# Optimization experiments

Hardware: AMD Instinct MI355X
Metric: run time of the kernel (lower is better)

## Reference

```python
import jax, jax.numpy as jnp
import numpy as np

L, B, DM, H, HID, NSPK, NB, NC, WIN = 128, 64, 1024, 256, 256, 2, 30, 6, 10
F = 2 * H            # biLSTM output feature dim
MEM = F + HID        # concat of node features and graph-conv output
R = 2 * NSPK * NSPK  # number of edge relations


def _build_edges():
    src_l, dst_l = [], []
    for j in range(L):
        for k in range(max(0, j - WIN), min(L, j + WIN + 1)):
            dst_l.append(j); src_l.append(k)
    dst = np.asarray(dst_l, np.int32); src = np.asarray(src_l, np.int32)
    offs = (np.arange(B, dtype=np.int32) * L)[:, None]
    edge_dst = (dst[None] + offs).reshape(-1)
    edge_src = (src[None] + offs).reshape(-1)
    mask = np.zeros((L, L), bool); mask[dst, src] = True
    return edge_src, edge_dst, mask


def setup_inputs():
    key = jax.random.key(0)
    ks = iter(jax.random.split(key, 32))
    rn = lambda *s: jax.random.normal(next(ks), s, jnp.float32) * 0.05
    edge_src, edge_dst, edge_mask = _build_edges()
    return {
        'U': jax.random.normal(next(ks), (L, B, DM), jnp.float32),
        'umask': jnp.ones((B, L), jnp.float32),
        'Wih0': rn(2, 4 * H, DM), 'Whh0': rn(2, 4 * H, H), 'b0': rn(2, 4 * H),
        'Wih1': rn(2, 4 * H, F), 'Whh1': rn(2, 4 * H, H), 'b1': rn(2, 4 * H),
        'W_scalar': rn(F, L),
        'basis': rn(NB, F, HID), 'comp': rn(R, NB),
        'W_root': rn(F, HID), 'b_rgcn': rn(HID),
        'gc_W1': rn(HID, HID), 'gc_W2': rn(HID, HID), 'gc_b': rn(HID),
        'Wm': rn(MEM, MEM), 'bm': rn(MEM),
        'Wl': rn(MEM, HID), 'bl': rn(HID),
        'Ws': rn(HID, NC), 'bs': rn(NC),
        'speakers': jax.random.randint(next(ks), (L, B), 0, NSPK, jnp.int32),
        'edge_src': jnp.asarray(edge_src), 'edge_dst': jnp.asarray(edge_dst),
        'edge_mask': jnp.asarray(edge_mask),
    }


def _lstm_dir(x, Wih, Whh, b, reverse):
    Bx, Hh = x.shape[1], Whh.shape[1]
    def step(carry, xt):
        h, c = carry
        g = xt @ Wih.T + h @ Whh.T + b          # PyTorch gate order i,f,g,o
        i, f, gg, o = jnp.split(g, 4, axis=-1)
        c = jax.nn.sigmoid(f) * c + jax.nn.sigmoid(i) * jnp.tanh(gg)
        h = jax.nn.sigmoid(o) * jnp.tanh(c)
        return (h, c), h
    init = (jnp.zeros((Bx, Hh), x.dtype), jnp.zeros((Bx, Hh), x.dtype))
    return jax.lax.scan(step, init, x, reverse=reverse)[1]


def _bilstm(x, Wih, Whh, b):
    return jnp.concatenate([_lstm_dir(x, Wih[0], Whh[0], b[0], False),
                            _lstm_dir(x, Wih[1], Whh[1], b[1], True)], -1)


def reference(U, umask, Wih0, Whh0, b0, Wih1, Whh1, b1, W_scalar, basis, comp,
              W_root, b_rgcn, gc_W1, gc_W2, gc_b, Wm, bm, Wl, bl, Ws, bs,
              speakers, edge_src, edge_dst, edge_mask):
    # --- 2-layer biLSTM encoder ---
    feats = _bilstm(_bilstm(U, Wih0, Whh0, b0), Wih1, Whh1, b1)   # (L,B,F)
    # --- MaskedEdgeAttention ('attn1'): edge weights ---
    scale = jnp.einsum('sbd,dm->sbm', feats, W_scalar)            # (L,B,L)
    alpha = jax.nn.softmax(scale, axis=0).transpose(1, 2, 0)      # (B,Lt,Ls)
    masked = alpha * jnp.where(edge_mask, 1.0, 1e-10)
    scores = masked / masked.sum(-1, keepdims=True) * edge_mask
    b_idx = edge_dst // L; i0 = edge_dst % L; i1 = edge_src % L
    edge_norm = scores[b_idx, i0, i1]                             # (E,)
    # --- edge types: speaker pair + temporal direction ---
    s_dst = speakers[i0, b_idx]; s_src = speakers[i1, b_idx]
    e_dir = jnp.where(i0 < i1, 0, 1)
    edge_type = s_dst * (2 * NSPK) + s_src * 2 + e_dir            # (E,) in [0,R)
    # --- node features, conversation-major ---
    x = feats.transpose(1, 0, 2).reshape(B * L, F)                # (N,F)
    N = B * L
    # --- RGCNConv with basis decomposition ---
    W_rel = jnp.einsum('rb,bfo->rfo', comp, basis)                # (R,F,HID)
    x_rel = jnp.einsum('nf,rfo->nro', x, W_rel)                   # (N,R,HID)
    msg = x_rel[edge_src, edge_type] * edge_norm[:, None]
    h = jax.ops.segment_sum(msg, edge_dst, num_segments=N) + x @ W_root + b_rgcn
    # --- GraphConv ---
    agg = jax.ops.segment_sum(h[edge_src], edge_dst, num_segments=N)
    h2 = h @ gc_W1 + gc_b + agg @ gc_W2                           # (N,HID)
    em = jnp.concatenate([x, h2], -1)                             # (N,MEM)
    em = em.reshape(B, L, MEM).transpose(1, 0, 2)                 # (L,B,MEM)
    # --- MatchingAttention ('general2') at every timestep, vectorized ---
    um = umask.T                                                  # (L,B)
    x_tr = em @ Wm + bm                                           # (L,B,MEM)
    logits = jnp.einsum('tbm,sbm->tbs', x_tr, em * um[:, :, None]) * umask[None]
    a = jax.nn.softmax(jnp.tanh(logits), axis=2) * umask[None]
    a = a / a.sum(2, keepdims=True)
    att = jnp.einsum('tbs,sbm->tbm', a, em)
    hidden = jax.nn.relu(att @ Wl + bl)                           # dropout = eval identity
    logp = jax.nn.log_softmax(hidden @ Ws + bs, axis=2)           # (L,B,NC)
    return logp.transpose(1, 0, 2).reshape(B * L, NC)
```

## Files before the change

### kernel.cpp

```cpp
#include <hip/hip_runtime.h>
#include <cstdint>


typedef __attribute__((ext_vector_type(8))) short bf16x8;
typedef __attribute__((ext_vector_type(4))) float f32x4;

__device__ __forceinline__ void gload_lds16(const void* g, void* l) {
  __builtin_amdgcn_global_load_lds(
      (const __attribute__((address_space(1))) void*)g,
      (__attribute__((address_space(3))) void*)l, 16, 0, 0);
}

template<bool HASBIAS, bool ACCUM, bool RELU, bool OUTBF>
__global__ __launch_bounds__(256) void gemm_bf16_nt(
    const ushort* __restrict__ A, const ushort* __restrict__ Bt,
    const float* __restrict__ bias, void* __restrict__ Cv,
    int M, int N, int K, long sA, long sB, long sC, long sBias)
{
  const int bz = blockIdx.z;
  A += (long)bz * sA;
  Bt += (long)bz * sB;
  if (HASBIAS) bias += (long)bz * sBias;
  float*  Cf = OUTBF ? nullptr : ((float*)Cv + (long)bz * sC);
  ushort* Cb = OUTBF ? ((ushort*)Cv + (long)bz * sC) : nullptr;

  const int bn = blockIdx.x * 128, bm = blockIdx.y * 128;

  __shared__ ushort As[128][32];
  __shared__ ushort Bs[128][32];

  const int tid = threadIdx.x;
  const int wave = tid >> 6, lane = tid & 63;
  const int wm = (wave >> 1) * 64, wn = (wave & 1) * 64;
  const int fr = lane & 15;
  const int fk = (lane >> 4) * 8;

  f32x4 acc[4][4];
#pragma unroll
  for (int i = 0; i < 4; ++i)
#pragma unroll
    for (int j = 0; j < 4; ++j) acc[i][j] = (f32x4){0.f, 0.f, 0.f, 0.f};

  const int f0 = wave * 2 * 64 + lane;
  const int f1 = f0 + 64;
  const int r0 = f0 >> 2, c0 = (f0 & 3) * 8;
  const int r1 = f1 >> 2, c1 = (f1 & 3) * 8;
  ushort* As0 = (ushort*)As + wave * 2 * 512;
  ushort* As1 = As0 + 512;
  ushort* Bs0 = (ushort*)Bs + wave * 2 * 512;
  ushort* Bs1 = Bs0 + 512;

  for (int k0 = 0; k0 < K; k0 += 32) {
    gload_lds16(A + (long)(bm + r0) * K + k0 + c0, As0);
    gload_lds16(A + (long)(bm + r1) * K + k0 + c1, As1);
    gload_lds16(Bt + (long)(bn + r0) * K + k0 + c0, Bs0);
    gload_lds16(Bt + (long)(bn + r1) * K + k0 + c1, Bs1);
    __syncthreads();

    bf16x8 af[4], bfr[4];
#pragma unroll
    for (int f = 0; f < 4; ++f) {
      af[f]  = *(const bf16x8*)&As[wm + f * 16 + fr][fk];
      bfr[f] = *(const bf16x8*)&Bs[wn + f * 16 + fr][fk];
    }
#pragma unroll
    for (int mf = 0; mf < 4; ++mf)
#pragma unroll
      for (int nf = 0; nf < 4; ++nf)
        acc[mf][nf] = __builtin_amdgcn_mfma_f32_16x16x32_bf16(
            af[mf], bfr[nf], acc[mf][nf], 0, 0, 0);
    __syncthreads();
  }

  float bv[4];
#pragma unroll
  for (int nf = 0; nf < 4; ++nf)
    bv[nf] = HASBIAS ? bias[bn + wn + nf * 16 + fr] : 0.f;

  const int crow0 = (lane >> 4) * 4;
#pragma unroll
  for (int mf = 0; mf < 4; ++mf)
#pragma unroll
    for (int r = 0; r < 4; ++r) {
      const long roff = (long)(bm + wm + mf * 16 + crow0 + r) * N + bn + wn;
#pragma unroll
      for (int nf = 0; nf < 4; ++nf) {
        float v = acc[mf][nf][r] + bv[nf];
        if (OUTBF) {
          unsigned u = __float_as_uint(v);
          u += 0x7fffu + ((u >> 16) & 1u);
          Cb[roff + nf * 16 + fr] = (ushort)(u >> 16);
        } else {
          if (ACCUM) v += Cf[roff + nf * 16 + fr];
          if (RELU) v = fmaxf(v, 0.f);
          Cf[roff + nf * 16 + fr] = v;
        }
      }
    }
}

__device__ __forceinline__ unsigned short f2bf(float f) {
  unsigned u = __float_as_uint(f);
  u += 0x7fffu + ((u >> 16) & 1u);
  return (unsigned short)(u >> 16);
}
__device__ __forceinline__ float bf2f(ushort v) {
  return __uint_as_float(((unsigned)v) << 16);
}
__device__ __forceinline__ float fast_sig(float x) {
  return __builtin_amdgcn_rcpf(1.f + __expf(-x));
}
__device__ __forceinline__ float fast_tanh(float x) {
  return 2.f * fast_sig(2.f * x) - 1.f;
}

__device__ __forceinline__ int sdot4_(uint a, uint b, int c) {
#if __has_builtin(__builtin_amdgcn_sdot4)
  return __builtin_amdgcn_sdot4((int)a, (int)b, c, false);
#else
  int r = c;
  r += ((int)(a << 24) >> 24) * ((int)(b << 24) >> 24);
  r += ((int)(a << 16) >> 24) * ((int)(b << 16) >> 24);
  r += ((int)(a << 8)  >> 24) * ((int)(b << 8)  >> 24);
  r += ((int)a >> 24)         * ((int)b >> 24);
  return r;
#endif
}

__global__ __launch_bounds__(256) void cvt_all_k(
    const float* __restrict__ U, ushort* __restrict__ ubf,
    const float* __restrict__ W0, ushort* __restrict__ w0,
    const float* __restrict__ W1, ushort* __restrict__ w1)
{
  const int bid = blockIdx.x;
  const float* src; ushort* dst; long base;
  if (bid < 8192)       { src = U;  dst = ubf; base = (long)bid * 1024; }
  else if (bid < 10240) { src = W0; dst = w0;  base = (long)(bid - 8192) * 1024; }
  else                  { src = W1; dst = w1;  base = (long)(bid - 10240) * 1024; }
  const long i = base + threadIdx.x * 4;
  float4 v = *(const float4*)(src + i);
  ushort4 o;
  o.x = f2bf(v.x); o.y = f2bf(v.y); o.z = f2bf(v.z); o.w = f2bf(v.w);
  *(ushort4*)(dst + i) = o;
}

__global__ __launch_bounds__(256) void tp_all_k(
    const float* __restrict__ s0, ushort* __restrict__ d0,
    const float* __restrict__ s1, ushort* __restrict__ d1,
    const float* __restrict__ s2, ushort* __restrict__ d2,
    const float* __restrict__ s3, ushort* __restrict__ d3,
    const float* __restrict__ s4, ushort* __restrict__ d4,
    const float* __restrict__ s5, ushort* __restrict__ d5)
{
  __shared__ float tile[32][33];
  const int bid = blockIdx.x;
  const float* src; ushort* dst; int R, C, gx, local;
  if (bid < 128)       { src = s0; dst = d0; R = 512; C = 256; gx = 8;  local = bid; }
  else if (bid < 192)  { src = s1; dst = d1; R = 256; C = 256; gx = 8;  local = bid - 128; }
  else if (bid < 256)  { src = s2; dst = d2; R = 256; C = 256; gx = 8;  local = bid - 192; }
  else if (bid < 832)  { src = s3; dst = d3; R = 768; C = 768; gx = 24; local = bid - 256; }
  else if (bid < 1024) { src = s4; dst = d4; R = 768; C = 256; gx = 8;  local = bid - 832; }
  else                 { src = s5; dst = d5; R = 512; C = 128; gx = 4;  local = bid - 1024; }
  const int c0 = (local % gx) * 32, r0 = (local / gx) * 32;
  const int tx = threadIdx.x & 31, ty = threadIdx.x >> 5;
#pragma unroll
  for (int j = 0; j < 4; ++j)
    tile[ty + j * 8][tx] = src[(long)(r0 + ty + j * 8) * C + c0 + tx];
  __syncthreads();
#pragma unroll
  for (int j = 0; j < 4; ++j)
    dst[(long)(c0 + ty + j * 8) * R + r0 + tx] = f2bf(tile[tx][ty + j * 8]);
}

__global__ __launch_bounds__(256) void pack_whh_all_k(
    const float* __restrict__ Whh0, const float* __restrict__ Whh1,
    uint* __restrict__ Wq, float* __restrict__ fscale)
{
  const int wid = (blockIdx.x * 256 + threadIdx.x) >> 6;
  const int lane = threadIdx.x & 63;
  const int l = wid >> 11;
  const int wid2 = wid & 2047;
  const int d = wid2 >> 10, gi = wid2 & 1023;
  const float* Whh = l ? Whh1 : Whh0;
  const float* row = Whh + ((long)d * 1024 + gi) * 256 + lane * 4;
  float v0 = row[0], v1 = row[1], v2 = row[2], v3 = row[3];
  float am = fmaxf(fmaxf(fabsf(v0), fabsf(v1)), fmaxf(fabsf(v2), fabsf(v3)));
#pragma unroll
  for (int off = 32; off > 0; off >>= 1) am = fmaxf(am, __shfl_xor(am, off, 64));
  am = fmaxf(am, 1e-12f);
  const float inv = 127.f / am;
  int q0 = __float2int_rn(v0 * inv), q1 = __float2int_rn(v1 * inv);
  int q2 = __float2int_rn(v2 * inv), q3 = __float2int_rn(v3 * inv);
  uint w = (uint)(q0 & 255) | ((uint)(q1 & 255) << 8) |
           ((uint)(q2 & 255) << 16) | ((uint)(q3 & 255) << 24);
  Wq[(long)l * 131072 + ((long)d * 64 + lane) * 1024 + gi] = w;
  if (lane == 0) fscale[l * 2048 + d * 1024 + gi] = am / 127.f;
}

__global__ __launch_bounds__(1024) void lstm4_k(
    const float* __restrict__ Xg,
    const uint* __restrict__ Wq,
    const float* __restrict__ fscale,
    ushort* __restrict__ out,
    int bmajor)
{
  const int bx = blockIdx.x;
  const int d = bx >> 6, b = bx & 63;
  const int tid = threadIdx.x;

  __shared__ uint hq[2][64];
  __shared__ float preactF[1024];

  uint w[64];
  const uint* wrow = Wq + (long)d * 65536 + tid;
#pragma unroll
  for (int k4 = 0; k4 < 64; ++k4) w[k4] = wrow[k4 * 1024];

  if (tid < 128) ((uint*)hq)[tid] = 0u;

  const float fsc = fscale[d * 1024 + tid] * (1.0f / 127.0f);
  const float* Xd = Xg + (long)d * 8192 * 1024;

  float c = 0.f;
  float x0 = 0.f, x1 = 0.f, x2 = 0.f, x3 = 0.f;
  if (tid < 256) {
    const float* xr = Xd + ((long)((d ? 127 : 0) * 64 + b)) * 1024;
    x0 = xr[tid]; x1 = xr[tid + 256]; x2 = xr[tid + 512]; x3 = xr[tid + 768];
  }
  __syncthreads();

  int cur = 0;
  for (int step = 0; step < 128; ++step) {
    const int t = d ? 127 - step : step;

    float n0 = 0.f, n1 = 0.f, n2 = 0.f, n3 = 0.f;
    if (tid < 256 && step + 1 < 128) {
      const float* xr = Xd + ((long)((d ? 126 - step : step + 1) * 64 + b)) * 1024;
      n0 = xr[tid]; n1 = xr[tid + 256]; n2 = xr[tid + 512]; n3 = xr[tid + 768];
    }

    int acc = 0;
    const uint4* hrow = (const uint4*)hq[cur];
#pragma unroll
    for (int k16 = 0; k16 < 16; ++k16) {
      uint4 h4 = hrow[k16];
      acc = sdot4_(w[k16 * 4 + 0], h4.x, acc);
      acc = sdot4_(w[k16 * 4 + 1], h4.y, acc);
      acc = sdot4_(w[k16 * 4 + 2], h4.z, acc);
      acc = sdot4_(w[k16 * 4 + 3], h4.w, acc);
    }
    preactF[tid] = (float)acc * fsc;
    __syncthreads();

    if (tid < 256) {
      float p0 = x0 + preactF[tid];
      float p1 = x1 + preactF[tid + 256];
      float p2 = x2 + preactF[tid + 512];
      float p3 = x3 + preactF[tid + 768];
      const float ig = fast_sig(p0), fg = fast_sig(p1);
      const float gg = fast_tanh(p2), og = fast_sig(p3);
      c = fg * c + ig * gg;
      const float h = og * fast_tanh(c);
      const long row = bmajor ? ((long)b * 128 + t) : ((long)t * 64 + b);
      out[row * 512 + (d << 8) + tid] = f2bf(h);
      ((char*)hq[cur ^ 1])[tid] = (char)__float2int_rn(h * 127.f);
      x0 = n0; x1 = n1; x2 = n2; x3 = n3;
    }
    __syncthreads();
    cur ^= 1;
  }
}

__global__ __launch_bounds__(256) void wrel_k(const float* __restrict__ basis,
                                              const float* __restrict__ comp,
                                              ushort* __restrict__ wrel2t) {
  const int f = blockIdx.x;
  const int o = threadIdx.x;
  __shared__ float cs[240];
  if (o < 240) cs[o] = comp[o];
  __syncthreads();
  float acc[8];
#pragma unroll
  for (int r = 0; r < 8; ++r) acc[r] = 0.f;
  for (int bb = 0; bb < 30; ++bb) {
    const float v = basis[((long)bb * 512 + f) * 256 + o];
#pragma unroll
    for (int r = 0; r < 8; ++r) acc[r] = fmaf(cs[r * 30 + bb], v, acc[r]);
  }
#pragma unroll
  for (int r = 0; r < 8; ++r)
    wrel2t[((long)(r * 256 + o)) * 512 + f] = f2bf(acc[r]);
}

__global__ __launch_bounds__(256) void rgcn_fused_k(
    const float* __restrict__ scale, const ushort* __restrict__ xrel,
    const float* __restrict__ hroot, const int* __restrict__ spk,
    ushort* __restrict__ hbf)
{
  const int n = blockIdx.x;
  const int b = n >> 7, t = n & 127;
  const int o = threadIdx.x;
  const int lo = max(t - 10, 0), hi = min(t + 10, 127);
  const int cnt = hi - lo + 1;

  __shared__ float sc[128], red[128];
  __shared__ int spks[21];
  __shared__ int spkt_s;

  if (o < 128) {
    const float v = scale[((long)(b * 128 + o)) * 128 + t];
    sc[o] = v; red[o] = v;
  }
  if (o == 0) spkt_s = spk[t * 64 + b];
  if (o >= 128 && o - 128 < cnt) spks[o - 128] = spk[(lo + o - 128) * 64 + b];
  __syncthreads();
  for (int off = 64; off > 0; off >>= 1) {
    if (o < off) red[o] = fmaxf(red[o], red[o + off]);
    __syncthreads();
  }
  const float m = red[0];
  __syncthreads();
  if (o < 128) {
    const float e = expf(sc[o] - m);
    sc[o] = e;
    const int dd = o - t;
    const bool inwin = (dd <= 10) && (dd >= -10);
    red[o] = e * (inwin ? 1.0f : 1e-10f);
  }
  __syncthreads();
  for (int off = 64; off > 0; off >>= 1) {
    if (o < off) red[o] += red[o + off];
    __syncthreads();
  }
  const float inv_msum = 1.0f / red[0];
  __syncthreads();

  const int spkt = spkt_s;
  float acc = hroot[(long)n * 256 + o];
  for (int q = 0; q < cnt; ++q) {
    const int s = lo + q;
    const float wv = sc[s] * inv_msum;
    const int et = spkt * 4 + spks[q] * 2 + ((t < s) ? 0 : 1);
    acc = fmaf(bf2f(xrel[(((long)(b * 128 + s)) * 8 + et) * 256 + o]), wv, acc);
  }
  hbf[(long)n * 256 + o] = f2bf(acc);
}

__global__ __launch_bounds__(256) void agg_k(const ushort* __restrict__ hbf,
                                             ushort* __restrict__ aggbf) {
  const int n = blockIdx.x;
  const int b = n >> 7, t = n & 127;
  const int o = threadIdx.x;
  const int lo = max(t - 10, 0), hi = min(t + 10, 127);
  float acc = 0.f;
  for (int s = lo; s <= hi; ++s) acc += bf2f(hbf[((long)(b * 128 + s)) * 256 + o]);
  aggbf[(long)n * 256 + o] = f2bf(acc);
}

__global__ __launch_bounds__(256) void em_k(const ushort* __restrict__ xbf,
                                            const float* __restrict__ h2,
                                            ushort* __restrict__ embf) {
  const int n = blockIdx.x;
  const int tid = threadIdx.x;
  embf[(long)n * 768 + tid] = xbf[(long)n * 512 + tid];
  embf[(long)n * 768 + 256 + tid] = xbf[(long)n * 512 + 256 + tid];
  embf[(long)n * 768 + 512 + tid] = f2bf(h2[(long)n * 256 + tid]);
}

__global__ __launch_bounds__(256) void emt_k(const ushort* __restrict__ src,
                                             ushort* __restrict__ dst) {
  __shared__ ushort tile[32][33];
  const int c0 = blockIdx.x * 32;
  const int r0 = blockIdx.y * 32;
  const int b = blockIdx.z;
  const ushort* s = src + (long)b * 98304;
  ushort* d = dst + (long)b * 98304;
  const int tx = threadIdx.x & 31, ty = threadIdx.x >> 5;
#pragma unroll
  for (int j = 0; j < 4; ++j)
    tile[ty + j * 8][tx] = s[(long)(r0 + ty + j * 8) * 768 + c0 + tx];
  __syncthreads();
#pragma unroll
  for (int j = 0; j < 4; ++j)
    d[(long)(c0 + ty + j * 8) * 128 + r0 + tx] = tile[tx][ty + j * 8];
}

__global__ __launch_bounds__(128) void match_softmax_k(const float* __restrict__ logits,
                                                       const float* __restrict__ umask,
                                                       ushort* __restrict__ abf) {
  const int bx = blockIdx.x;
  const int b = bx >> 7;
  const int s = threadIdx.x;
  __shared__ float red[128];
  const float* row = logits + (long)bx * 128;
  const float um = umask[b * 128 + s];
  const float v = tanhf(row[s] * um * um);
  red[s] = v; __syncthreads();
  for (int off = 64; off > 0; off >>= 1) { if (s < off) red[s] = fmaxf(red[s], red[s + off]); __syncthreads(); }
  const float m = red[0]; __syncthreads();
  const float e = expf(v - m);
  red[s] = e; __syncthreads();
  for (int off = 64; off > 0; off >>= 1) { if (s < off) red[s] += red[s + off]; __syncthreads(); }
  const float es = red[0]; __syncthreads();
  const float p = (e / es) * um;
  red[s] = p; __syncthreads();
  for (int off = 64; off > 0; off >>= 1) { if (s < off) red[s] += red[s + off]; __syncthreads(); }
  const float ps = red[0];
  abf[(long)bx * 128 + s] = f2bf(p / ps);
}

__global__ __launch_bounds__(256) void final_k(const float* __restrict__ hidden,
                                               const float* __restrict__ Ws,
                                               const float* __restrict__ bs,
                                               float* __restrict__ out) {
  __shared__ float wsl[256 * 6];
  const int tid = threadIdx.x;
#pragma unroll
  for (int j = 0; j < 6; ++j) wsl[tid * 6 + j] = Ws[tid * 6 + j];
  __syncthreads();
  const int wave = tid >> 6, lane = tid & 63;
  const int n = blockIdx.x * 4 + wave;
  const float4 hv = *(const float4*)&hidden[(long)n * 256 + lane * 4];
  const float hvv[4] = {hv.x, hv.y, hv.z, hv.w};
  float a[6];
#pragma unroll
  for (int c = 0; c < 6; ++c) a[c] = 0.f;
#pragma unroll
  for (int j = 0; j < 4; ++j)
#pragma unroll
    for (int c = 0; c < 6; ++c)
      a[c] = fmaf(hvv[j], wsl[(lane * 4 + j) * 6 + c], a[c]);
#pragma unroll
  for (int off = 32; off > 0; off >>= 1)
#pragma unroll
    for (int c = 0; c < 6; ++c)
      a[c] += __shfl_xor(a[c], off, 64);
  if (lane == 0) {
    float v[6], m = -1e30f;
#pragma unroll
    for (int c = 0; c < 6; ++c) { v[c] = a[c] + bs[c]; m = fmaxf(m, v[c]); }
    float sum = 0.f;
#pragma unroll
    for (int c = 0; c < 6; ++c) sum += expf(v[c] - m);
    const float lse = m + logf(sum);
#pragma unroll
    for (int c = 0; c < 6; ++c) out[(long)n * 6 + c] = v[c] - lse;
  }
}

extern "C" void kernel_launch(void* const* d_in, const int* in_sizes, int n_in,
                              void* d_out, int out_size, void* d_ws, size_t ws_size,
                              hipStream_t stream) {
  const float* U        = (const float*)d_in[0];
  const float* umask    = (const float*)d_in[1];
  const float* Wih0     = (const float*)d_in[2];
  const float* Whh0     = (const float*)d_in[3];
  const float* b0       = (const float*)d_in[4];
  const float* Wih1     = (const float*)d_in[5];
  const float* Whh1     = (const float*)d_in[6];
  const float* b1       = (const float*)d_in[7];
  const float* W_scalar = (const float*)d_in[8];
  const float* basis    = (const float*)d_in[9];
  const float* comp     = (const float*)d_in[10];
  const float* W_root   = (const float*)d_in[11];
  const float* b_rgcn   = (const float*)d_in[12];
  const float* gc_W1    = (const float*)d_in[13];
  const float* gc_W2    = (const float*)d_in[14];
  const float* gc_b     = (const float*)d_in[15];
  const float* Wm       = (const float*)d_in[16];
  const float* bm       = (const float*)d_in[17];
  const float* Wl       = (const float*)d_in[18];
  const float* bl       = (const float*)d_in[19];
  const float* Wsw      = (const float*)d_in[20];
  const float* bsw      = (const float*)d_in[21];
  const int*   speakers = (const int*)d_in[22];

  float* ws = (float*)d_ws;
  float* gates   = ws + 0L;
  float* feats   = ws + 16777216L;
  float* xbuf    = ws + 20971520L;
  float* feats0  = ws + 25165824L;
  float* scaleb  = ws + 29360128L;
  float* scoresb = ws + 30408704L;
  float* wrelr   = ws + 31457280L;
  float* hroot   = ws + 32505856L;
  uint*  wq      = (uint*)(ws + 34603008L);
  float* fsc     = ws + 34865152L;
  float* wTr     = ws + 34869248L;

  ushort* ubf    = (ushort*)xbuf;
  ushort* wih0bf = (ushort*)feats;
  ushort* wih1bf = (ushort*)(feats + 1048576L);
  ushort* f0bf   = (ushort*)feats0;
  ushort* xbf    = (ushort*)xbuf;
  ushort* wrel2t = (ushort*)wrelr;
  ushort* wroott = (ushort*)wTr;
  ushort* gcW1t  = wroott + 131072L;
  ushort* gcW2t  = gcW1t + 65536L;
  ushort* Wmt    = gcW2t + 65536L;
  ushort* Wlt    = Wmt + 589824L;
  ushort* wscT   = (ushort*)scoresb;

  ushort* hbf     = (ushort*)(feats0 + 2097152L);
  ushort* aggbf   = (ushort*)(feats0 + 3145728L);
  ushort* embf    = (ushort*)feats0;
  ushort* emT     = (ushort*)xbuf;
  ushort* xrelbf  = (ushort*)gates;
  ushort* xtrbf   = (ushort*)gates;
  ushort* abf     = (ushort*)scoresb;
  ushort* attbf   = (ushort*)feats;

  float*  h2b     = hroot;
  float*  logitsb = scaleb;
  float*  hiddenb = scaleb;

  pack_whh_all_k<<<1024, 256, 0, stream>>>(Whh0, Whh1, wq, fsc);
  cvt_all_k<<<11264, 256, 0, stream>>>(U, ubf, Wih0, wih0bf, Wih1, wih1bf);
  tp_all_k<<<1088, 256, 0, stream>>>(W_root, wroott, gc_W1, gcW1t, gc_W2, gcW2t,
                                     Wm, Wmt, Wl, Wlt, W_scalar, wscT);
  wrel_k<<<512, 256, 0, stream>>>(basis, comp, wrel2t);

  gemm_bf16_nt<true, false, false, false><<<dim3(8, 64, 2), 256, 0, stream>>>(
      ubf, wih0bf, b0, gates, 8192, 1024, 1024, 0L, 1048576L, 8388608L, 1024L);
  lstm4_k<<<128, 1024, 0, stream>>>(gates, wq, fsc, f0bf, 0);

  gemm_bf16_nt<true, false, false, false><<<dim3(8, 64, 2), 256, 0, stream>>>(
      f0bf, wih1bf, b1, gates, 8192, 1024, 512, 0L, 524288L, 8388608L, 1024L);
  lstm4_k<<<128, 1024, 0, stream>>>(gates, wq + 131072, fsc + 2048, xbf, 1);

  gemm_bf16_nt<false, false, false, false><<<dim3(1, 64, 1), 256, 0, stream>>>(
      xbf, wscT, nullptr, scaleb, 8192, 128, 512, 0L, 0L, 0L, 0L);
  gemm_bf16_nt<true, false, false, false><<<dim3(2, 64, 1), 256, 0, stream>>>(
      xbf, wroott, b_rgcn, hroot, 8192, 256, 512, 0L, 0L, 0L, 0L);
  gemm_bf16_nt<false, false, false, true><<<dim3(16, 64, 1), 256, 0, stream>>>(
      xbf, wrel2t, nullptr, xrelbf, 8192, 2048, 512, 0L, 0L, 0L, 0L);
  rgcn_fused_k<<<8192, 256, 0, stream>>>(scaleb, xrelbf, hroot, speakers, hbf);

  agg_k<<<8192, 256, 0, stream>>>(hbf, aggbf);
  gemm_bf16_nt<true, false, false, false><<<dim3(2, 64, 1), 256, 0, stream>>>(
      hbf, gcW1t, gc_b, h2b, 8192, 256, 256, 0L, 0L, 0L, 0L);
  gemm_bf16_nt<false, true, false, false><<<dim3(2, 64, 1), 256, 0, stream>>>(
      aggbf, gcW2t, nullptr, h2b, 8192, 256, 256, 0L, 0L, 0L, 0L);

  em_k<<<8192, 256, 0, stream>>>(xbf, h2b, embf);
  gemm_bf16_nt<true, false, false, true><<<dim3(6, 64, 1), 256, 0, stream>>>(
      embf, Wmt, bm, xtrbf, 8192, 768, 768, 0L, 0L, 0L, 0L);
  emt_k<<<dim3(24, 4, 64), 256, 0, stream>>>(embf, emT);
  gemm_bf16_nt<false, false, false, false><<<dim3(1, 1, 64), 256, 0, stream>>>(
      xtrbf, embf, nullptr, logitsb, 128, 128, 768, 98304L, 98304L, 16384L, 0L);
  match_softmax_k<<<8192, 128, 0, stream>>>(logitsb, umask, abf);
  gemm_bf16_nt<false, false, false, true><<<dim3(6, 1, 64), 256, 0, stream>>>(
      abf, emT, nullptr, attbf, 128, 768, 128, 16384L, 98304L, 98304L, 0L);

  gemm_bf16_nt<true, false, true, false><<<dim3(2, 64, 1), 256, 0, stream>>>(
      attbf, Wlt, bl, hiddenb, 8192, 256, 768, 0L, 0L, 0L, 0L);
  final_k<<<2048, 256, 0, stream>>>(hiddenb, Wsw, bsw, (float*)d_out);
}
```

Measured before the change: 623.6 us.

## Write LSTM and GraphConv outputs in place into strided concat buffer

Adds separate lda/ldc strides to the GEMM so operands and outputs can live inside a wider row-major buffer. The second LSTM now writes straight into the first 512 columns of the 768-wide memory buffer. The GraphConv output GEMM writes bf16 into the last 256 columns, which removes the em_k concat kernel. The two GraphConv GEMMs are merged into one K=512 GEMM over an interleaved [h | agg] buffer with stacked transposed weights, dropping one launch and the fp32 read-modify-write accumulate. The trade-off is strided A loads and a GraphConv output rounded to bf16 before it is reused.

After: 611.1 us (median of 2 runs). -2.0%, faster.

```diff
diff --git a/kernel.cpp b/kernel.cpp
--- a/kernel.cpp
+++ b/kernel.cpp
@@ -15,7 +15,8 @@
 __global__ __launch_bounds__(256) void gemm_bf16_nt(
     const ushort* __restrict__ A, const ushort* __restrict__ Bt,
     const float* __restrict__ bias, void* __restrict__ Cv,
-    int M, int N, int K, long sA, long sB, long sC, long sBias)
+    int M, int N, int K, long lda, long ldc,
+    long sA, long sB, long sC, long sBias)
 {
   const int bz = blockIdx.z;
   A += (long)bz * sA;
@@ -51,8 +52,8 @@
   ushort* Bs1 = Bs0 + 512;
 
   for (int k0 = 0; k0 < K; k0 += 32) {
-    gload_lds16(A + (long)(bm + r0) * K + k0 + c0, As0);
-    gload_lds16(A + (long)(bm + r1) * K + k0 + c1, As1);
+    gload_lds16(A + (long)(bm + r0) * lda + k0 + c0, As0);
+    gload_lds16(A + (long)(bm + r1) * lda + k0 + c1, As1);
     gload_lds16(Bt + (long)(bn + r0) * K + k0 + c0, Bs0);
     gload_lds16(Bt + (long)(bn + r1) * K + k0 + c1, Bs1);
     __syncthreads();
@@ -82,7 +83,7 @@
   for (int mf = 0; mf < 4; ++mf)
 #pragma unroll
     for (int r = 0; r < 4; ++r) {
-      const long roff = (long)(bm + wm + mf * 16 + crow0 + r) * N + bn + wn;
+      const long roff = (long)(bm + wm + mf * 16 + crow0 + r) * ldc + bn + wn;
 #pragma unroll
       for (int nf = 0; nf < 4; ++nf) {
         float v = acc[mf][nf][r] + bv[nf];
@@ -146,21 +147,21 @@
 
 __global__ __launch_bounds__(256) void tp_all_k(
     const float* __restrict__ s0, ushort* __restrict__ d0,
-    const float* __restrict__ s1, ushort* __restrict__ d1,
-    const float* __restrict__ s2, ushort* __restrict__ d2,
+    const float* __restrict__ s1, const float* __restrict__ s2,
+    ushort* __restrict__ d12,
     const float* __restrict__ s3, ushort* __restrict__ d3,
     const float* __restrict__ s4, ushort* __restrict__ d4,
     const float* __restrict__ s5, ushort* __restrict__ d5)
 {
   __shared__ float tile[32][33];
   const int bid = blockIdx.x;
-  const float* src; ushort* dst; int R, C, gx, local;
-  if (bid < 128)       { src = s0; dst = d0; R = 512; C = 256; gx = 8;  local = bid; }
-  else if (bid < 192)  { src = s1; dst = d1; R = 256; C = 256; gx = 8;  local = bid - 128; }
-  else if (bid < 256)  { src = s2; dst = d2; R = 256; C = 256; gx = 8;  local = bid - 192; }
-  else if (bid < 832)  { src = s3; dst = d3; R = 768; C = 768; gx = 24; local = bid - 256; }
-  else if (bid < 1024) { src = s4; dst = d4; R = 768; C = 256; gx = 8;  local = bid - 832; }
-  else                 { src = s5; dst = d5; R = 512; C = 128; gx = 4;  local = bid - 1024; }
+  const float* src; ushort* dst; int C, gx, local, dstStride, dstOff;
+  if (bid < 128)       { src = s0; dst = d0;  C = 256; gx = 8;  local = bid;        dstStride = 512; dstOff = 0; }
+  else if (bid < 192)  { src = s1; dst = d12; C = 256; gx = 8;  local = bid - 128;  dstStride = 512; dstOff = 0; }
+  else if (bid < 256)  { src = s2; dst = d12; C = 256; gx = 8;  local = bid - 192;  dstStride = 512; dstOff = 256; }
+  else if (bid < 832)  { src = s3; dst = d3;  C = 768; gx = 24; local = bid - 256;  dstStride = 768; dstOff = 0; }
+  else if (bid < 1024) { src = s4; dst = d4;  C = 256; gx = 8;  local = bid - 832;  dstStride = 768; dstOff = 0; }
+  else                 { src = s5; dst = d5;  C = 128; gx = 4;  local = bid - 1024; dstStride = 512; dstOff = 0; }
   const int c0 = (local % gx) * 32, r0 = (local / gx) * 32;
   const int tx = threadIdx.x & 31, ty = threadIdx.x >> 5;
 #pragma unroll
@@ -169,7 +170,7 @@
   __syncthreads();
 #pragma unroll
   for (int j = 0; j < 4; ++j)
-    dst[(long)(c0 + ty + j * 8) * R + r0 + tx] = f2bf(tile[tx][ty + j * 8]);
+    dst[(long)(c0 + ty + j * 8) * dstStride + dstOff + r0 + tx] = f2bf(tile[tx][ty + j * 8]);
 }
 
 __global__ __launch_bounds__(256) void pack_whh_all_k(
@@ -202,7 +203,7 @@
     const uint* __restrict__ Wq,
     const float* __restrict__ fscale,
     ushort* __restrict__ out,
-    int bmajor)
+    int bmajor, long ldo)
 {
   const int bx = blockIdx.x;
   const int d = bx >> 6, b = bx & 63;
@@ -262,7 +263,7 @@
       c = fg * c + ig * gg;
       const float h = og * fast_tanh(c);
       const long row = bmajor ? ((long)b * 128 + t) : ((long)t * 64 + b);
-      out[row * 512 + (d << 8) + tid] = f2bf(h);
+      out[row * ldo + (d << 8) + tid] = f2bf(h);
       ((char*)hq[cur ^ 1])[tid] = (char)__float2int_rn(h * 127.f);
       x0 = n0; x1 = n1; x2 = n2; x3 = n3;
     }
@@ -295,7 +296,7 @@
 __global__ __launch_bounds__(256) void rgcn_fused_k(
     const float* __restrict__ scale, const ushort* __restrict__ xrel,
     const float* __restrict__ hroot, const int* __restrict__ spk,
-    ushort* __restrict__ hbf)
+    ushort* __restrict__ hagg)
 {
   const int n = blockIdx.x;
   const int b = n >> 7, t = n & 127;
@@ -343,28 +344,17 @@
     const int et = spkt * 4 + spks[q] * 2 + ((t < s) ? 0 : 1);
     acc = fmaf(bf2f(xrel[(((long)(b * 128 + s)) * 8 + et) * 256 + o]), wv, acc);
   }
-  hbf[(long)n * 256 + o] = f2bf(acc);
-}
-
-__global__ __launch_bounds__(256) void agg_k(const ushort* __restrict__ hbf,
-                                             ushort* __restrict__ aggbf) {
+  hagg[(long)n * 512 + o] = f2bf(acc);
+}
+
+__global__ __launch_bounds__(256) void agg_k(ushort* __restrict__ hagg) {
   const int n = blockIdx.x;
   const int b = n >> 7, t = n & 127;
   const int o = threadIdx.x;
   const int lo = max(t - 10, 0), hi = min(t + 10, 127);
   float acc = 0.f;
-  for (int s = lo; s <= hi; ++s) acc += bf2f(hbf[((long)(b * 128 + s)) * 256 + o]);
-  aggbf[(long)n * 256 + o] = f2bf(acc);
-}
-
-__global__ __launch_bounds__(256) void em_k(const ushort* __restrict__ xbf,
-                                            const float* __restrict__ h2,
-                                            ushort* __restrict__ embf) {
-  const int n = blockIdx.x;
-  const int tid = threadIdx.x;
-  embf[(long)n * 768 + tid] = xbf[(long)n * 512 + tid];
-  embf[(long)n * 768 + 256 + tid] = xbf[(long)n * 512 + 256 + tid];
-  embf[(long)n * 768 + 512 + tid] = f2bf(h2[(long)n * 256 + tid]);
+  for (int s = lo; s <= hi; ++s) acc += bf2f(hagg[((long)(b * 128 + s)) * 512 + o]);
+  hagg[(long)n * 512 + 256 + o] = f2bf(acc);
 }
 
 __global__ __launch_bounds__(256) void emt_k(const ushort* __restrict__ src,
@@ -492,67 +482,64 @@
   ushort* wih0bf = (ushort*)feats;
   ushort* wih1bf = (ushort*)(feats + 1048576L);
   ushort* f0bf   = (ushort*)feats0;
-  ushort* xbf    = (ushort*)xbuf;
+  ushort* xemb   = (ushort*)feats0;
   ushort* wrel2t = (ushort*)wrelr;
   ushort* wroott = (ushort*)wTr;
-  ushort* gcW1t  = wroott + 131072L;
-  ushort* gcW2t  = gcW1t + 65536L;
-  ushort* Wmt    = gcW2t + 65536L;
+  ushort* gcW12t = wroott + 131072L;
+  ushort* Wmt    = gcW12t + 131072L;
   ushort* Wlt    = Wmt + 589824L;
   ushort* wscT   = (ushort*)scoresb;
 
-  ushort* hbf     = (ushort*)(feats0 + 2097152L);
-  ushort* aggbf   = (ushort*)(feats0 + 3145728L);
-  ushort* embf    = (ushort*)feats0;
+  ushort* hagg    = (ushort*)xbuf;
   ushort* emT     = (ushort*)xbuf;
   ushort* xrelbf  = (ushort*)gates;
   ushort* xtrbf   = (ushort*)gates;
   ushort* abf     = (ushort*)scoresb;
   ushort* attbf   = (ushort*)feats;
 
-  float*  h2b     = hroot;
   float*  logitsb = scaleb;
   float*  hiddenb = scaleb;
 
   pack_whh_all_k<<<1024, 256, 0, stream>>>(Whh0, Whh1, wq, fsc);
   cvt_all_k<<<11264, 256, 0, stream>>>(U, ubf, Wih0, wih0bf, Wih1, wih1bf);
-  tp_all_k<<<1088, 256, 0, stream>>>(W_root, wroott, gc_W1, gcW1t, gc_W2, gcW2t,
+  tp_all_k<<<1088, 256, 0, stream>>>(W_root, wroott, gc_W1, gc_W2, gcW12t,
                                      Wm, Wmt, Wl, Wlt, W_scalar, wscT);
   wrel_k<<<512, 256, 0, stream>>>(basis, comp, wrel2t);
 
   gemm_bf16_nt<true, false, false, false><<<dim3(8, 64, 2), 256, 0, stream>>>(
-      ubf, wih0bf, b0, gates, 8192, 1024, 1024, 0L, 1048576L, 8388608L, 1024L);
-  lstm4_k<<<128, 1024, 0, stream>>>(gates, wq, fsc, f0bf, 0);
+      ubf, wih0bf, b0, gates, 8192, 1024, 1024, 1024L, 1024L,
+      0L, 1048576L, 8388608L, 1024L);
+  lstm4_k<<<128, 1024, 0, stream>>>(gates, wq, fsc, f0bf, 0, 512L);
 
   gemm_bf16_nt<true, false, false, false><<<dim3(8, 64, 2), 256, 0, stream>>>(
-      f0bf, wih1bf, b1, gates, 8192, 1024, 512, 0L, 524288L, 8388608L, 1024L);
-  lstm4_k<<<128, 1024, 0, stream>>>(gates, wq + 131072, fsc + 2048, xbf, 1);
+      f0bf, wih1bf, b1, gates, 8192, 1024, 512, 512L, 1024L,
+      0L, 524288L, 8388608L, 1024L);
+  lstm4_k<<<128, 1024, 0, stream>>>(gates, wq + 131072, fsc + 2048, xemb, 1, 768L);
 
   gemm_bf16_nt<false, false, false, false><<<dim3(1, 64, 1), 256, 0, stream>>>(
-      xbf, wscT, nullptr, scaleb, 8192, 128, 512, 0L, 0L, 0L, 0L);
+      xemb, wscT, nullptr, scaleb, 8192, 128, 512, 768L, 128L, 0L, 0L, 0L, 0L);
   gemm_bf16_nt<true, false, false, false><<<dim3(2, 64, 1), 256, 0, stream>>>(
-      xbf, wroott, b_rgcn, hroot, 8192, 256, 512, 0L, 0L, 0L, 0L);
+      xemb, wroott, b_rgcn, hroot, 8192, 256, 512, 768L, 256L, 0L, 0L, 0L, 0L);
   gemm_bf16_nt<false, false, false, true><<<dim3(16, 64, 1), 256, 0, stream>>>(
-      xbf, wrel2t, nullptr, xrelbf, 8192, 2048, 512, 0L, 0L, 0L, 0L);
-  rgcn_fused_k<<<8192, 256, 0, stream>>>(scaleb, xrelbf, hroot, speakers, hbf);
-
-  agg_k<<<8192, 256, 0, stream>>>(hbf, aggbf);
-  gemm_bf16_nt<true, false, false, false><<<dim3(2, 64, 1), 256, 0, stream>>>(
-      hbf, gcW1t, gc_b, h2b, 8192, 256, 256, 0L, 0L, 0L, 0L);
-  gemm_bf16_nt<false, true, false, false><<<dim3(2, 64, 1), 256, 0, stream>>>(
-      aggbf, gcW2t, nullptr, h2b, 8192, 256, 256, 0L, 0L, 0L, 0L);
-
-  em_k<<<8192, 256, 0, stream>>>(xbf, h2b, embf);
+      xemb, wrel2t, nullptr, xrelbf, 8192, 2048, 512, 768L, 2048L, 0L, 0L, 0L, 0L);
+  rgcn_fused_k<<<8192, 256, 0, stream>>>(scaleb, xrelbf, hroot, speakers, hagg);
+
+  agg_k<<<8192, 256, 0, stream>>>(hagg);
+  gemm_bf16_nt<true, false, false, true><<<dim3(2, 64, 1), 256, 0, stream>>>(
+      hagg, gcW12t, gc_b, xemb + 512, 8192, 256, 512, 512L, 768L, 0L, 0L, 0L, 0L);
+
   gemm_bf16_nt<true, false, false, true><<<dim3(6, 64, 1), 256, 0, stream>>>(
-      embf, Wmt, bm, xtrbf, 8192, 768, 768, 0L, 0L, 0L, 0L);
-  emt_k<<<dim3(24, 4, 64), 256, 0, stream>>>(embf, emT);
+      xemb, Wmt, bm, xtrbf, 8192, 768, 768, 768L, 768L, 0L, 0L, 0L, 0L);
+  emt_k<<<dim3(24, 4, 64), 256, 0, stream>>>(xemb, emT);
   gemm_bf16_nt<false, false, false, false><<<dim3(1, 1, 64), 256, 0, stream>>>(
-      xtrbf, embf, nullptr, logitsb, 128, 128, 768, 98304L, 98304L, 16384L, 0L);
+      xtrbf, xemb, nullptr, logitsb, 128, 128, 768, 768L, 128L,
+      98304L, 98304L, 16384L, 0L);
   match_softmax_k<<<8192, 128, 0, stream>>>(logitsb, umask, abf);
   gemm_bf16_nt<false, false, false, true><<<dim3(6, 1, 64), 256, 0, stream>>>(
-      abf, emT, nullptr, attbf, 128, 768, 128, 16384L, 98304L, 98304L, 0L);
+      abf, emT, nullptr, attbf, 128, 768, 128, 128L, 768L,
+      16384L, 98304L, 98304L, 0L);
 
   gemm_bf16_nt<true, false, true, false><<<dim3(2, 64, 1), 256, 0, stream>>>(
-      attbf, Wlt, bl, hiddenb, 8192, 256, 768, 0L, 0L, 0L, 0L);
+      attbf, Wlt, bl, hiddenb, 8192, 256, 768, 768L, 256L, 0L, 0L, 0L, 0L);
   final_k<<<2048, 256, 0, stream>>>(hiddenb, Wsw, bsw, (float*)d_out);
 }
```
